# Performance work log

Hardware: AMD Instinct MI355X
Metric: run time of the kernel (lower is better)

The kernel has to match this reference:

```python
import jax, jax.numpy as jnp
import numpy as np

B, T, D = 4, 2048, 768
D_CONV, D_GRIF, D_FFN, K = 384, 384, 2048, 3
EPS = 1e-6


def rmsnorm(x, w):
    rms = jax.lax.rsqrt(jnp.mean(jnp.square(x.astype(jnp.float32)), axis=-1, keepdims=True) + EPS)
    return (x.astype(jnp.float32) * rms).astype(x.dtype) * w


def causal_dwconv(x, w):
    # x: [B,T,C], w: [C,K] depthwise causal conv
    k = w.shape[1]
    xp = jnp.pad(x, ((0, 0), (k - 1, 0), (0, 0)))  # left pad -> causal
    out = jax.lax.conv_general_dilated(
        xp.transpose(0, 2, 1), w[:, None, :],  # [B,C,T+K-1], [C,1,K]
        window_strides=(1,), padding='VALID',
        dimension_numbers=('NCW', 'OIW', 'NCW'),
        feature_group_count=w.shape[0])
    return out.transpose(0, 2, 1)  # [B,T,C]


def rg_lru(v, r, i, lam):
    # Griffin RG-LRU: log_a = -8*softplus(lam)*r; h_t = a*h_{t-1} + sqrt(1-a^2)*(i*v)
    log_a = -8.0 * jax.nn.softplus(lam) * r                # [B,T,Dg]
    a = jnp.exp(log_a)
    gated = jnp.sqrt(jnp.maximum(1.0 - jnp.exp(2.0 * log_a), EPS)) * (i * v)
    def comb(c1, c2):
        a1, b1 = c1
        a2, b2 = c2
        return (a1 * a2, a2 * b1 + b2)
    _, h = jax.lax.associative_scan(comb, (a, gated), axis=1)
    return h


def setup_inputs() -> dict:
    key = jax.random.key(0)
    ks = jax.random.split(key, 16)
    s_in = 1.0 / np.sqrt(D)
    s_ffn = 1.0 / np.sqrt(D_FFN)
    return {
        'x': jax.random.normal(ks[0], (B, T, D), jnp.float32),
        'velocity': jnp.zeros((B, T, D), jnp.float32),
        'pre_norm_w': jnp.ones((D,), jnp.float32),
        'conv_in_w': jax.random.normal(ks[1], (D, 2 * D_CONV), jnp.float32) * s_in,
        'conv_dw_w': jax.random.normal(ks[2], (D_CONV, K), jnp.float32) * (1.0 / np.sqrt(K)),
        'grif_v_w': jax.random.normal(ks[3], (D, D_GRIF), jnp.float32) * s_in,
        'grif_r_w': jax.random.normal(ks[4], (D, D_GRIF), jnp.float32) * s_in,
        'grif_i_w': jax.random.normal(ks[5], (D, D_GRIF), jnp.float32) * s_in,
        'grif_lam': jax.random.uniform(ks[6], (D_GRIF,), jnp.float32, 0.5, 2.0),
        'out_w': jax.random.normal(ks[7], (D, D), jnp.float32) * s_in,
        'log_beta': jnp.array(0.0, jnp.float32),  # log(0.5/(1-0.5))
        'ffn_norm_w': jnp.ones((D,), jnp.float32),
        'w1': jax.random.normal(ks[8], (D, D_FFN), jnp.float32) * s_in,
        'w3': jax.random.normal(ks[9], (D, D_FFN), jnp.float32) * s_in,
        'w2': jax.random.normal(ks[10], (D_FFN, D), jnp.float32) * s_ffn,
    }


def reference(x, velocity, pre_norm_w, conv_in_w, conv_dw_w, grif_v_w, grif_r_w,
              grif_i_w, grif_lam, out_w, log_beta, ffn_norm_w, w1, w3, w2):
    xn = rmsnorm(x, pre_norm_w)
    # GatedConv branch -> [B,T,D_CONV]
    u, g = jnp.split(xn @ conv_in_w, 2, axis=-1)
    conv_out = causal_dwconv(u, conv_dw_w) * jax.nn.silu(g)
    # Griffin RG-LRU branch -> [B,T,D_GRIF]
    v = xn @ grif_v_w
    r = jax.nn.sigmoid(xn @ grif_r_w)
    i = jax.nn.sigmoid(xn @ grif_i_w)
    griffin_out = rg_lru(v, r, i, grif_lam)
    # concat -> out_proj -> momentum residual
    mixer_out = jnp.concatenate([conv_out, griffin_out], axis=-1) @ out_w
    beta = jax.nn.sigmoid(log_beta)
    velocity = beta * velocity + mixer_out
    x = x + velocity
    # ffn: RMSNorm -> SwiGLU -> residual
    normed = rmsnorm(x, ffn_norm_w)
    x = x + (jax.nn.silu(normed @ w1) * (normed @ w3)) @ w2
    return (x, velocity)
```

## Files before the change

kernel.cpp:

```cpp
#include <hip/hip_runtime.h>
#include <hip/hip_bf16.h>
#include <cstdint>

#define BSZ   4
#define TSEQ  2048
#define DMOD  768
#define DCONV 384
#define DGRIF 384
#define DFFN  2048
#define BT    (BSZ*TSEQ)
#define NG1   1920
#define G1LD  2048
#define EPS_  1e-6f

typedef __bf16 bf16;
typedef __bf16 bf16x8 __attribute__((ext_vector_type(8)));
typedef float  f32x4  __attribute__((ext_vector_type(4)));

__device__ __forceinline__ float sigmoidf_(float x) { return 1.f / (1.f + __expf(-x)); }

__device__ __forceinline__ void gload_lds16(const void* g, void* l) {
  __builtin_amdgcn_global_load_lds(
      (const __attribute__((address_space(1))) void*)(uintptr_t)g,
      (__attribute__((address_space(3))) void*)(uint32_t)(uintptr_t)l,
      16, 0, 0);
}

__device__ __forceinline__ int swz_wg() {
  const int nwg = gridDim.x;
  const int bid = blockIdx.x;
  const int cpx = nwg >> 3;
  return (bid & 7) * cpx + (bid >> 3);
}

#define SBAR() __builtin_amdgcn_s_barrier()
#define VMCNT6() asm volatile("s_waitcnt vmcnt(6)" ::: "memory")
#define VMCNT4() asm volatile("s_waitcnt vmcnt(4)" ::: "memory")
#define VMCNT0() asm volatile("s_waitcnt vmcnt(0)" ::: "memory")

template <int EPI>
__global__ __launch_bounds__(512, 2) void gemm256(
    const bf16* __restrict__ A, const bf16* __restrict__ Bt, bf16* __restrict__ C,
    int K, int nx, int ldc)
{
  extern __shared__ __align__(16) char lds_dyn[];

  const int wg = swz_wg();
  const int m0 = (wg / nx) * 256;
  const int bx = wg % nx;
  const int n0 = bx * 256;
  const int tid  = threadIdx.x;
  const int lane = tid & 63;
  const int wr = (tid >> 6) >> 2;
  const int wc = (tid >> 6) & 3;
  const int lr = lane & 15;
  const int lk4 = lane >> 4;

  f32x4 acc[8][4] = {};
  bf16x8 af[4], bfr[4];

  const int nt = K >> 6;

  auto ldA = [&](int cur, int kk, int row) -> bf16x8 {
    const int off = (cur << 15) + (kk << 14) + row * 64 + ((lk4 ^ ((row >> 1) & 3)) << 4);
    return *reinterpret_cast<const bf16x8*>(&lds_dyn[off]);
  };
  auto ldB = [&](int cur, int kk, int row) -> bf16x8 {
    const int off = 65536 + (cur << 15) + (kk << 14) + row * 64 + ((lk4 ^ ((row >> 1) & 3)) << 4);
    return *reinterpret_cast<const bf16x8*>(&lds_dyn[off]);
  };
  auto stageA = [&](int t, int kk) {
    const bf16* g = A + (size_t)m0 * K + t * 64 + kk * 32;
    const int dstbase = ((t & 1) << 15) + (kk << 14);
    #pragma unroll
    for (int p = 0; p < 2; ++p) {
      const int f = (p << 9) + tid;
      const int row = f >> 2;
      const int gs = (f & 3) ^ ((row >> 1) & 3);
      gload_lds16(g + (size_t)row * K + gs * 8,
                  &lds_dyn[dstbase + (p << 13) + ((tid >> 6) << 10)]);
    }
  };
  auto stageB = [&](int t, int kk) {
    const bf16* g = Bt + (size_t)n0 * K + t * 64 + kk * 32;
    const int dstbase = 65536 + ((t & 1) << 15) + (kk << 14);
    #pragma unroll
    for (int p = 0; p < 2; ++p) {
      const int f = (p << 9) + tid;
      const int row = f >> 2;
      const int gs = (f & 3) ^ ((row >> 1) & 3);
      gload_lds16(g + (size_t)row * K + gs * 8,
                  &lds_dyn[dstbase + (p << 13) + ((tid >> 6) << 10)]);
    }
  };

  stageA(0, 0); stageB(0, 0); stageA(0, 1); stageB(0, 1); stageA(1, 0);
  VMCNT6();
  SBAR();

  for (int t = 0; t < nt; ++t) {
    const int cur = t & 1;
    const bool s1 = (t + 1 < nt), s2 = (t + 2 < nt);

    #pragma unroll
    for (int i = 0; i < 4; ++i) af[i] = ldA(cur, 0, wr * 128 + i * 16 + lr);
    #pragma unroll
    for (int i = 0; i < 4; ++i) bfr[i] = ldB(cur, 0, wc * 64 + i * 16 + lr);
    if (s1) stageB(t + 1, 0);
    SBAR();
    __builtin_amdgcn_s_setprio(1);
    #pragma unroll
    for (int mi = 0; mi < 4; ++mi)
      #pragma unroll
      for (int ni = 0; ni < 4; ++ni)
        acc[mi][ni] = __builtin_amdgcn_mfma_f32_16x16x32_bf16(af[mi], bfr[ni], acc[mi][ni], 0, 0, 0);
    __builtin_amdgcn_s_setprio(0);
    SBAR();

    #pragma unroll
    for (int i = 0; i < 4; ++i) af[i] = ldA(cur, 0, wr * 128 + 64 + i * 16 + lr);
    if (s1) stageA(t + 1, 1);
    SBAR();
    __builtin_amdgcn_s_setprio(1);
    #pragma unroll
    for (int mi = 0; mi < 4; ++mi)
      #pragma unroll
      for (int ni = 0; ni < 4; ++ni)
        acc[4 + mi][ni] = __builtin_amdgcn_mfma_f32_16x16x32_bf16(af[mi], bfr[ni], acc[4 + mi][ni], 0, 0, 0);
    __builtin_amdgcn_s_setprio(0);
    if (s1) { VMCNT6(); } else { VMCNT0(); }
    SBAR();

    #pragma unroll
    for (int i = 0; i < 4; ++i) af[i] = ldA(cur, 1, wr * 128 + i * 16 + lr);
    #pragma unroll
    for (int i = 0; i < 4; ++i) bfr[i] = ldB(cur, 1, wc * 64 + i * 16 + lr);
    if (s1) stageB(t + 1, 1);
    SBAR();
    __builtin_amdgcn_s_setprio(1);
    #pragma unroll
    for (int mi = 0; mi < 4; ++mi)
      #pragma unroll
      for (int ni = 0; ni < 4; ++ni)
        acc[mi][ni] = __builtin_amdgcn_mfma_f32_16x16x32_bf16(af[mi], bfr[ni], acc[mi][ni], 0, 0, 0);
    __builtin_amdgcn_s_setprio(0);
    SBAR();

    #pragma unroll
    for (int i = 0; i < 4; ++i) af[i] = ldA(cur, 1, wr * 128 + 64 + i * 16 + lr);
    if (s2) stageA(t + 2, 0);
    SBAR();
    __builtin_amdgcn_s_setprio(1);
    #pragma unroll
    for (int mi = 0; mi < 4; ++mi)
      #pragma unroll
      for (int ni = 0; ni < 4; ++ni)
        acc[4 + mi][ni] = __builtin_amdgcn_mfma_f32_16x16x32_bf16(af[mi], bfr[ni], acc[4 + mi][ni], 0, 0, 0);
    __builtin_amdgcn_s_setprio(0);
    if (s2) { VMCNT6(); } else if (s1) { VMCNT4(); }
    SBAR();
  }

  if (EPI == 0) {
    #pragma unroll
    for (int a = 0; a < 8; ++a)
      #pragma unroll
      for (int ni = 0; ni < 4; ++ni)
        #pragma unroll
        for (int reg = 0; reg < 4; ++reg) {
          const int r = m0 + wr * 128 + a * 16 + lk4 * 4 + reg;
          const int c = n0 + wc * 64 + ni * 16 + lr;
          C[(size_t)r * ldc + c] = (bf16)acc[a][ni][reg];
        }
  } else {
    char* comb = lds_dyn;
    const int q = wc >> 1;
    if (wc & 1) {
      #pragma unroll
      for (int a = 0; a < 8; ++a)
        #pragma unroll
        for (int ni = 0; ni < 4; ++ni)
          #pragma unroll
          for (int reg = 0; reg < 4; ++reg) {
            const int r = wr * 128 + a * 16 + lk4 * 4 + reg;
            const int col = ni * 16 + lr;
            *reinterpret_cast<bf16*>(&comb[(q << 15) + r * 128 + col * 2]) = (bf16)acc[a][ni][reg];
          }
    }
    SBAR();
    if (!(wc & 1)) {
      #pragma unroll
      for (int a = 0; a < 8; ++a)
        #pragma unroll
        for (int ni = 0; ni < 4; ++ni)
          #pragma unroll
          for (int reg = 0; reg < 4; ++reg) {
            const int r = wr * 128 + a * 16 + lk4 * 4 + reg;
            const int col = ni * 16 + lr;
            const float p3 = (float)*reinterpret_cast<const bf16*>(&comb[(q << 15) + r * 128 + col * 2]);
            const float p1 = acc[a][ni][reg];
            C[(size_t)(m0 + r) * ldc + (bx * 2 + q) * 64 + col] = (bf16)(p1 * sigmoidf_(p1) * p3);
          }
    }
  }
}

template <int MODE>
__global__ __launch_bounds__(256) void transpose_bf16_kernel(
    const float* __restrict__ W, bf16* __restrict__ Wt, int R, int C, int Cpad, int half)
{
  __shared__ float tile[32][33];
  const int tc = blockIdx.x * 32;
  const int tr = blockIdx.y * 32;
  const int lx = threadIdx.x;
  const int ly = threadIdx.y;
  #pragma unroll
  for (int i = ly; i < 32; i += 8) {
    int r = tr + i, c = tc + lx;
    tile[i][lx] = (r < R && c < C) ? W[(size_t)r * C + c] : 0.f;
  }
  __syncthreads();
  #pragma unroll
  for (int i = ly; i < 32; i += 8) {
    int oc = tc + i;
    int orr = tr + lx;
    if (orr < R) {
      if (MODE == 0) {
        if (oc < Cpad) Wt[(size_t)oc * R + orr] = (bf16)tile[lx][i];
      } else {
        if (oc < C) {
          int orow = ((oc >> 6) << 7) + half + (oc & 63);
          Wt[(size_t)orow * R + orr] = (bf16)tile[lx][i];
        }
      }
    }
  }
}

__global__ __launch_bounds__(256) void rmsnorm_kernel(
    const float* __restrict__ x, const float* __restrict__ w, bf16* __restrict__ out)
{
  __shared__ float sbuf[4];
  const int row = blockIdx.x;
  const int tid = threadIdx.x;
  const float* xr = x + (size_t)row * DMOD;
  float v0 = xr[tid], v1 = xr[tid + 256], v2 = xr[tid + 512];
  float s = v0*v0 + v1*v1 + v2*v2;
  #pragma unroll
  for (int o = 32; o > 0; o >>= 1) s += __shfl_down(s, o, 64);
  if ((tid & 63) == 0) sbuf[tid >> 6] = s;
  __syncthreads();
  float tot = sbuf[0] + sbuf[1] + sbuf[2] + sbuf[3];
  float rms = rsqrtf(tot * (1.f / (float)DMOD) + EPS_);
  bf16* orow = out + (size_t)row * DMOD;
  orow[tid]       = (bf16)(v0 * rms * w[tid]);
  orow[tid + 256] = (bf16)(v1 * rms * w[tid + 256]);
  orow[tid + 512] = (bf16)(v2 * rms * w[tid + 512]);
}

template <int EPI>
__global__ __launch_bounds__(256) void gemm_n64(
    const bf16* __restrict__ A, const bf16* __restrict__ Bt, float* __restrict__ C,
    const float* __restrict__ xin, const float* __restrict__ vin,
    float* __restrict__ outv, const float* __restrict__ log_beta,
    int M, int N, int K, int nx)
{
  __shared__ alignas(16) unsigned short As[128 * 64];
  __shared__ alignas(16) unsigned short Bs[64 * 64];

  const int wg = swz_wg();
  const int m0 = (wg / nx) * 128, n0 = (wg % nx) * 64;
  const int tid  = threadIdx.x;
  const int wave = tid >> 6;
  const int lane = tid & 63;
  const int wr = wave >> 1, wc = wave & 1;

  f32x4 acc[4][2] = {};
  const int srow = lane >> 3;
  const int scol = ((lane & 7) ^ srow) * 8;
  const int lr = lane & 15;
  const int lsw = lr & 7;
  const int lk4 = lane >> 4;

  for (int k0 = 0; k0 < K; k0 += 64) {
    __syncthreads();
    #pragma unroll
    for (int it = 0; it < 6; ++it) {
      const int chunk = wave * 6 + it;
      if (chunk < 16) {
        const int row = chunk * 8 + srow;
        gload_lds16(A + (size_t)(m0 + row) * K + k0 + scol, (char*)As + chunk * 1024);
      } else {
        const int row = (chunk - 16) * 8 + srow;
        gload_lds16(Bt + (size_t)(n0 + row) * K + k0 + scol, (char*)Bs + (chunk - 16) * 1024);
      }
    }
    __syncthreads();
    #pragma unroll
    for (int kk = 0; kk < 2; ++kk) {
      bf16x8 af[4], bfr[2];
      #pragma unroll
      for (int i = 0; i < 4; ++i)
        af[i] = *reinterpret_cast<const bf16x8*>(
            &As[(wr*64 + i*16 + lr) * 64 + (((kk*4 + lk4) ^ lsw) * 8)]);
      #pragma unroll
      for (int i = 0; i < 2; ++i)
        bfr[i] = *reinterpret_cast<const bf16x8*>(
            &Bs[(wc*32 + i*16 + lr) * 64 + (((kk*4 + lk4) ^ lsw) * 8)]);
      #pragma unroll
      for (int mi = 0; mi < 4; ++mi)
        #pragma unroll
        for (int ni = 0; ni < 2; ++ni)
          acc[mi][ni] = __builtin_amdgcn_mfma_f32_16x16x32_bf16(af[mi], bfr[ni], acc[mi][ni], 0, 0, 0);
    }
  }

  const float beta = (EPI == 0) ? sigmoidf_(log_beta[0]) : 0.f;
  #pragma unroll
  for (int mi = 0; mi < 4; ++mi)
    #pragma unroll
    for (int ni = 0; ni < 2; ++ni)
      #pragma unroll
      for (int reg = 0; reg < 4; ++reg) {
        const int r = m0 + wr*64 + mi*16 + (lane >> 4) * 4 + reg;
        const int c = n0 + wc*32 + ni*16 + (lane & 15);
        const size_t off = (size_t)r * N + c;
        float v = acc[mi][ni][reg];
        if (EPI == 0) {
          float vel = beta * vin[off] + v;
          float x1  = xin[off] + vel;
          outv[off] = vel;
          C[off] = x1;
        } else {
          C[off] += v;
        }
      }
}

#define NCH  32
#define CLEN 64

__device__ __forceinline__ void lru_step(const bf16* row, int c, float coef,
                                         float& a, float& g)
{
  float v  = (float)row[2*DCONV + c];
  float r  = sigmoidf_((float)row[2*DCONV + DGRIF + c]);
  float is = sigmoidf_((float)row[2*DCONV + 2*DGRIF + c]);
  float la = coef * r;
  a = __expf(la);
  g = sqrtf(fmaxf(1.f - __expf(2.f * la), EPS_)) * (is * v);
}

__global__ __launch_bounds__(256) void lru_pass1(
    const bf16* __restrict__ g1, const float* __restrict__ lam,
    float* __restrict__ cA, float* __restrict__ cB)
{
  const int idx = blockIdx.x * 256 + threadIdx.x;
  const int c = idx % DGRIF;
  const int rest = idx / DGRIF;
  const int j = rest & (NCH - 1);
  const int b = rest / NCH;
  const float coef = -8.f * log1pf(__expf(lam[c]));
  const bf16* base = g1 + (size_t)(b * TSEQ + j * CLEN) * G1LD;
  float A = 1.f, Bv = 0.f;
  #pragma unroll 4
  for (int t = 0; t < CLEN; ++t) {
    float a, g;
    lru_step(base + (size_t)t * G1LD, c, coef, a, g);
    A *= a;
    Bv = a * Bv + g;
  }
  cA[((size_t)b * DGRIF + c) * NCH + j] = A;
  cB[((size_t)b * DGRIF + c) * NCH + j] = Bv;
}

__global__ __launch_bounds__(256) void lru_pass2(
    const bf16* __restrict__ g1, const float* __restrict__ lam,
    const float* __restrict__ cA, const float* __restrict__ cB,
    const float* __restrict__ dw, bf16* __restrict__ mixin)
{
  const int idx = blockIdx.x * 256 + threadIdx.x;
  const int c = idx % DGRIF;
  const int rest = idx / DGRIF;
  const int j = rest & (NCH - 1);
  const int b = rest / NCH;
  const float coef = -8.f * log1pf(__expf(lam[c]));
  float Hc = 0.f;
  const float* pa = cA + ((size_t)b * DGRIF + c) * NCH;
  const float* pb = cB + ((size_t)b * DGRIF + c) * NCH;
  for (int k = 0; k < j; ++k) Hc = pa[k] * Hc + pb[k];

  const int t0 = j * CLEN;
  const bf16* base = g1 + (size_t)(b * TSEQ + t0) * G1LD;
  const float w0 = dw[c*3], w1 = dw[c*3 + 1], w2 = dw[c*3 + 2];
  float u1 = (t0 >= 1) ? (float)base[-(ptrdiff_t)G1LD + c]     : 0.f;
  float u0 = (t0 >= 2) ? (float)base[-(ptrdiff_t)(2*G1LD) + c] : 0.f;

  bf16* mbase = mixin + (size_t)(b * TSEQ + t0) * DMOD;
  #pragma unroll 4
  for (int t = 0; t < CLEN; ++t) {
    const bf16* row = base + (size_t)t * G1LD;
    float u2 = (float)row[c];
    float gg = (float)row[DCONV + c];
    float conv = u0 * w0 + u1 * w1 + u2 * w2;
    mbase[(size_t)t * DMOD + c] = (bf16)(conv * (gg * sigmoidf_(gg)));
    u0 = u1; u1 = u2;
    float a, g;
    lru_step(row, c, coef, a, g);
    Hc = a * Hc + g;
    mbase[(size_t)t * DMOD + DCONV + c] = (bf16)Hc;
  }
}

extern "C" void kernel_launch(void* const* d_in, const int* in_sizes, int n_in,
                              void* d_out, int out_size, void* d_ws, size_t ws_size,
                              hipStream_t stream)
{
  const float* x         = (const float*)d_in[0];
  const float* vel_in    = (const float*)d_in[1];
  const float* pre_w     = (const float*)d_in[2];
  const float* conv_in_w = (const float*)d_in[3];
  const float* conv_dw   = (const float*)d_in[4];
  const float* gv        = (const float*)d_in[5];
  const float* gr        = (const float*)d_in[6];
  const float* gi        = (const float*)d_in[7];
  const float* lam       = (const float*)d_in[8];
  const float* out_w     = (const float*)d_in[9];
  const float* log_beta  = (const float*)d_in[10];
  const float* ffn_w     = (const float*)d_in[11];
  const float* w1        = (const float*)d_in[12];
  const float* w3        = (const float*)d_in[13];
  const float* w2        = (const float*)d_in[14];

  char* ws = (char*)d_ws;
  size_t off = 0;
  auto alloc = [&](size_t bytes) { void* p = ws + off; off += (bytes + 255) & ~(size_t)255; return p; };

  bf16*  WT_G1  = (bf16*)alloc((size_t)G1LD * DMOD * 2);
  bf16*  WT_OUT = (bf16*)alloc((size_t)DMOD * DMOD * 2);
  bf16*  WT_W13 = (bf16*)alloc((size_t)2 * DFFN * DMOD * 2);
  bf16*  WT_W2  = (bf16*)alloc((size_t)DMOD * DFFN * 2);
  float* CA     = (float*)alloc((size_t)BSZ * DGRIF * NCH * 4);
  float* CB     = (float*)alloc((size_t)BSZ * DGRIF * NCH * 4);
  bf16*  XN     = (bf16*)alloc((size_t)BT * DMOD * 2);
  bf16*  G1     = (bf16*)alloc((size_t)BT * G1LD * 2);
  bf16*  MIXIN  = (bf16*)alloc((size_t)BT * DMOD * 2);
  bf16*  H      = (bf16*)alloc((size_t)BT * DFFN * 2);
  bf16*  NORMED = (bf16*)alloc((size_t)BT * DMOD * 2);

  float* OUTX   = (float*)d_out;
  float* OUTV   = OUTX + (size_t)BT * DMOD;

  hipFuncSetAttribute((const void*)gemm256<0>, hipFuncAttributeMaxDynamicSharedMemorySize, 131072);
  hipFuncSetAttribute((const void*)gemm256<1>, hipFuncAttributeMaxDynamicSharedMemorySize, 131072);

  const dim3 tb(32, 8);
  hipMemsetAsync(WT_G1 + (size_t)NG1 * DMOD, 0, (size_t)(G1LD - NG1) * DMOD * 2, stream);
  transpose_bf16_kernel<0><<<dim3(DMOD/32,  DMOD/32), tb, 0, stream>>>(conv_in_w, WT_G1, DMOD, DMOD, DMOD, 0);
  transpose_bf16_kernel<0><<<dim3(DGRIF/32, DMOD/32), tb, 0, stream>>>(gv, WT_G1 + (size_t)(2*DCONV) * DMOD, DMOD, DGRIF, DGRIF, 0);
  transpose_bf16_kernel<0><<<dim3(DGRIF/32, DMOD/32), tb, 0, stream>>>(gr, WT_G1 + (size_t)(2*DCONV + DGRIF) * DMOD, DMOD, DGRIF, DGRIF, 0);
  transpose_bf16_kernel<0><<<dim3(DGRIF/32, DMOD/32), tb, 0, stream>>>(gi, WT_G1 + (size_t)(2*DCONV + 2*DGRIF) * DMOD, DMOD, DGRIF, DGRIF, 0);
  transpose_bf16_kernel<0><<<dim3(DMOD/32,  DMOD/32), tb, 0, stream>>>(out_w, WT_OUT, DMOD, DMOD, DMOD, 0);
  transpose_bf16_kernel<1><<<dim3(DFFN/32,  DMOD/32), tb, 0, stream>>>(w1, WT_W13, DMOD, DFFN, DFFN, 0);
  transpose_bf16_kernel<1><<<dim3(DFFN/32,  DMOD/32), tb, 0, stream>>>(w3, WT_W13, DMOD, DFFN, DFFN, 64);
  transpose_bf16_kernel<0><<<dim3(DMOD/32,  DFFN/32), tb, 0, stream>>>(w2, WT_W2, DFFN, DMOD, DMOD, 0);

  rmsnorm_kernel<<<BT, 256, 0, stream>>>(x, pre_w, XN);

  gemm256<0><<<(BT/256) * (G1LD/256), 512, 131072, stream>>>(XN, WT_G1, G1, DMOD, G1LD/256, G1LD);

  lru_pass1<<<(BSZ * NCH * DGRIF) / 256, 256, 0, stream>>>(G1, lam, CA, CB);
  lru_pass2<<<(BSZ * NCH * DGRIF) / 256, 256, 0, stream>>>(G1, lam, CA, CB, conv_dw, MIXIN);

  gemm_n64<0><<<(DMOD/64) * (BT/128), 256, 0, stream>>>(MIXIN, WT_OUT, OUTX, x, vel_in, OUTV,
                                                        log_beta, BT, DMOD, DMOD, DMOD/64);

  rmsnorm_kernel<<<BT, 256, 0, stream>>>(OUTX, ffn_w, NORMED);

  gemm256<1><<<(BT/256) * (2*DFFN/256), 512, 131072, stream>>>(NORMED, WT_W13, H, DMOD, 2*DFFN/256, DFFN);

  gemm_n64<1><<<(DMOD/64) * (BT/128), 256, 0, stream>>>(H, WT_W2, OUTX, nullptr, nullptr, nullptr,
                                                        nullptr, BT, DMOD, DFFN, DMOD/64);
}
```

Measured before the change: 290.9 us.

## Widen N-tile of output GEMMs to 128 and reorder gemm256 prefetch staging

The two narrow output GEMMs (out_proj and w2) now compute 128x128 tiles instead of 128x64. This halves the number of workgroups and reuses each A tile across twice as many columns, at the cost of more accumulator registers and fewer blocks to hide latency. Separately, the gemm256 pipeline now prefetches one more B stage up front and reorders the stageA/stageB issue points, waiting on vmcnt(8) instead of 6. That keeps more loads in flight ahead of the MFMA work.

```diff
diff --git a/kernel.cpp b/kernel.cpp
--- a/kernel.cpp
+++ b/kernel.cpp
@@ -34,9 +34,9 @@
 }
 
 #define SBAR() __builtin_amdgcn_s_barrier()
-#define VMCNT6() asm volatile("s_waitcnt vmcnt(6)" ::: "memory")
-#define VMCNT4() asm volatile("s_waitcnt vmcnt(4)" ::: "memory")
-#define VMCNT0() asm volatile("s_waitcnt vmcnt(0)" ::: "memory")
+#define VM8() asm volatile("s_waitcnt vmcnt(8)" ::: "memory")
+#define VM4() asm volatile("s_waitcnt vmcnt(4)" ::: "memory")
+#define VM0() asm volatile("s_waitcnt vmcnt(0)" ::: "memory")
 
 template <int EPI>
 __global__ __launch_bounds__(512, 2) void gemm256(
@@ -94,8 +94,8 @@
     }
   };
 
-  stageA(0, 0); stageB(0, 0); stageA(0, 1); stageB(0, 1); stageA(1, 0);
-  VMCNT6();
+  stageA(0, 0); stageB(0, 0); stageA(0, 1); stageB(0, 1); stageA(1, 0); stageB(1, 0);
+  VM8();
   SBAR();
 
   for (int t = 0; t < nt; ++t) {
@@ -106,7 +106,7 @@
     for (int i = 0; i < 4; ++i) af[i] = ldA(cur, 0, wr * 128 + i * 16 + lr);
     #pragma unroll
     for (int i = 0; i < 4; ++i) bfr[i] = ldB(cur, 0, wc * 64 + i * 16 + lr);
-    if (s1) stageB(t + 1, 0);
+    if (s1) stageA(t + 1, 1);
     SBAR();
     __builtin_amdgcn_s_setprio(1);
     #pragma unroll
@@ -119,7 +119,7 @@
 
     #pragma unroll
     for (int i = 0; i < 4; ++i) af[i] = ldA(cur, 0, wr * 128 + 64 + i * 16 + lr);
-    if (s1) stageA(t + 1, 1);
+    if (s1) stageB(t + 1, 1);
     SBAR();
     __builtin_amdgcn_s_setprio(1);
     #pragma unroll
@@ -128,14 +128,14 @@
       for (int ni = 0; ni < 4; ++ni)
         acc[4 + mi][ni] = __builtin_amdgcn_mfma_f32_16x16x32_bf16(af[mi], bfr[ni], acc[4 + mi][ni], 0, 0, 0);
     __builtin_amdgcn_s_setprio(0);
-    if (s1) { VMCNT6(); } else { VMCNT0(); }
+    if (s1) { VM8(); } else { VM0(); }
     SBAR();
 
     #pragma unroll
     for (int i = 0; i < 4; ++i) af[i] = ldA(cur, 1, wr * 128 + i * 16 + lr);
     #pragma unroll
     for (int i = 0; i < 4; ++i) bfr[i] = ldB(cur, 1, wc * 64 + i * 16 + lr);
-    if (s1) stageB(t + 1, 1);
+    if (s2) stageA(t + 2, 0);
     SBAR();
     __builtin_amdgcn_s_setprio(1);
     #pragma unroll
@@ -148,7 +148,7 @@
 
     #pragma unroll
     for (int i = 0; i < 4; ++i) af[i] = ldA(cur, 1, wr * 128 + 64 + i * 16 + lr);
-    if (s2) stageA(t + 2, 0);
+    if (s2) stageB(t + 2, 0);
     SBAR();
     __builtin_amdgcn_s_setprio(1);
     #pragma unroll
@@ -157,7 +157,7 @@
       for (int ni = 0; ni < 4; ++ni)
         acc[4 + mi][ni] = __builtin_amdgcn_mfma_f32_16x16x32_bf16(af[mi], bfr[ni], acc[4 + mi][ni], 0, 0, 0);
     __builtin_amdgcn_s_setprio(0);
-    if (s2) { VMCNT6(); } else if (s1) { VMCNT4(); }
+    if (s2) { VM8(); } else if (s1) { VM4(); }
     SBAR();
   }
 
@@ -259,23 +259,23 @@
 }
 
 template <int EPI>
-__global__ __launch_bounds__(256) void gemm_n64(
-    const bf16* __restrict__ A, const bf16* __restrict__ Bt, float* __restrict__ C,
+__global__ __launch_bounds__(256) void gemm_w128(
+    const bf16* __restrict__ A, const bf16* __restrict__ Bt, float* __restrict__ Cf,
     const float* __restrict__ xin, const float* __restrict__ vin,
     float* __restrict__ outv, const float* __restrict__ log_beta,
     int M, int N, int K, int nx)
 {
   __shared__ alignas(16) unsigned short As[128 * 64];
-  __shared__ alignas(16) unsigned short Bs[64 * 64];
+  __shared__ alignas(16) unsigned short Bs[128 * 64];
 
   const int wg = swz_wg();
-  const int m0 = (wg / nx) * 128, n0 = (wg % nx) * 64;
+  const int m0 = (wg / nx) * 128, n0 = (wg % nx) * 128;
   const int tid  = threadIdx.x;
   const int wave = tid >> 6;
   const int lane = tid & 63;
   const int wr = wave >> 1, wc = wave & 1;
 
-  f32x4 acc[4][2] = {};
+  f32x4 acc[4][4] = {};
   const int srow = lane >> 3;
   const int scol = ((lane & 7) ^ srow) * 8;
   const int lr = lane & 15;
@@ -285,54 +285,50 @@
   for (int k0 = 0; k0 < K; k0 += 64) {
     __syncthreads();
     #pragma unroll
-    for (int it = 0; it < 6; ++it) {
-      const int chunk = wave * 6 + it;
-      if (chunk < 16) {
-        const int row = chunk * 8 + srow;
-        gload_lds16(A + (size_t)(m0 + row) * K + k0 + scol, (char*)As + chunk * 1024);
-      } else {
-        const int row = (chunk - 16) * 8 + srow;
-        gload_lds16(Bt + (size_t)(n0 + row) * K + k0 + scol, (char*)Bs + (chunk - 16) * 1024);
-      }
+    for (int it = 0; it < 4; ++it) {
+      const int chunk = wave * 4 + it;
+      const int row = chunk * 8 + srow;
+      gload_lds16(A  + (size_t)(m0 + row) * K + k0 + scol, (char*)As + chunk * 1024);
+      gload_lds16(Bt + (size_t)(n0 + row) * K + k0 + scol, (char*)Bs + chunk * 1024);
     }
     __syncthreads();
     #pragma unroll
     for (int kk = 0; kk < 2; ++kk) {
-      bf16x8 af[4], bfr[2];
+      bf16x8 af[4], bfr[4];
       #pragma unroll
       for (int i = 0; i < 4; ++i)
         af[i] = *reinterpret_cast<const bf16x8*>(
             &As[(wr*64 + i*16 + lr) * 64 + (((kk*4 + lk4) ^ lsw) * 8)]);
       #pragma unroll
-      for (int i = 0; i < 2; ++i)
+      for (int i = 0; i < 4; ++i)
         bfr[i] = *reinterpret_cast<const bf16x8*>(
-            &Bs[(wc*32 + i*16 + lr) * 64 + (((kk*4 + lk4) ^ lsw) * 8)]);
+            &Bs[(wc*64 + i*16 + lr) * 64 + (((kk*4 + lk4) ^ lsw) * 8)]);
       #pragma unroll
       for (int mi = 0; mi < 4; ++mi)
         #pragma unroll
-        for (int ni = 0; ni < 2; ++ni)
+        for (int ni = 0; ni < 4; ++ni)
           acc[mi][ni] = __builtin_amdgcn_mfma_f32_16x16x32_bf16(af[mi], bfr[ni], acc[mi][ni], 0, 0, 0);
     }
   }
 
-  const float beta = (EPI == 0) ? sigmoidf_(log_beta[0]) : 0.f;
+  const float beta = (EPI == 1) ? sigmoidf_(log_beta[0]) : 0.f;
   #pragma unroll
   for (int mi = 0; mi < 4; ++mi)
     #pragma unroll
-    for (int ni = 0; ni < 2; ++ni)
+    for (int ni = 0; ni < 4; ++ni)
       #pragma unroll
       for (int reg = 0; reg < 4; ++reg) {
-        const int r = m0 + wr*64 + mi*16 + (lane >> 4) * 4 + reg;
-        const int c = n0 + wc*32 + ni*16 + (lane & 15);
+        const int r = m0 + wr*64 + mi*16 + lk4 * 4 + reg;
+        const int c = n0 + wc*64 + ni*16 + lr;
         const size_t off = (size_t)r * N + c;
         float v = acc[mi][ni][reg];
-        if (EPI == 0) {
+        if (EPI == 1) {
           float vel = beta * vin[off] + v;
           float x1  = xin[off] + vel;
           outv[off] = vel;
-          C[off] = x1;
+          Cf[off] = x1;
         } else {
-          C[off] += v;
+          Cf[off] += v;
         }
       }
 }
@@ -472,13 +468,13 @@
   lru_pass1<<<(BSZ * NCH * DGRIF) / 256, 256, 0, stream>>>(G1, lam, CA, CB);
   lru_pass2<<<(BSZ * NCH * DGRIF) / 256, 256, 0, stream>>>(G1, lam, CA, CB, conv_dw, MIXIN);
 
-  gemm_n64<0><<<(DMOD/64) * (BT/128), 256, 0, stream>>>(MIXIN, WT_OUT, OUTX, x, vel_in, OUTV,
-                                                        log_beta, BT, DMOD, DMOD, DMOD/64);
+  gemm_w128<1><<<(DMOD/128) * (BT/128), 256, 0, stream>>>(MIXIN, WT_OUT, OUTX, x, vel_in, OUTV,
+                                                          log_beta, BT, DMOD, DMOD, DMOD/128);
 
   rmsnorm_kernel<<<BT, 256, 0, stream>>>(OUTX, ffn_w, NORMED);
 
   gemm256<1><<<(BT/256) * (2*DFFN/256), 512, 131072, stream>>>(NORMED, WT_W13, H, DMOD, 2*DFFN/256, DFFN);
 
-  gemm_n64<1><<<(DMOD/64) * (BT/128), 256, 0, stream>>>(H, WT_W2, OUTX, nullptr, nullptr, nullptr,
-                                                        nullptr, BT, DMOD, DFFN, DMOD/64);
-}
+  gemm_w128<2><<<(DMOD/128) * (BT/128), 256, 0, stream>>>(H, WT_W2, OUTX, nullptr, nullptr, nullptr,
+                                                          nullptr, BT, DMOD, DFFN, DMOD/128);
+}
```

New measurement: 288.3 us. About the same (-0.9%).
